# Optimization experiments

Measured on AMD Instinct MI355X. Metric: run time of the kernel, lower is better.

Reference implementation:

```python
import jax, jax.numpy as jnp
import numpy as np

HIDDEN = 4096
N_HEADS = 32
N_KV = 8
HEAD_DIM = 128
ROPE_THETA = 10000.0
B, S = 2, 2048


def _rope_neox(x, cos, sin):
    # x: [B,S,H,D]; cos/sin: [B,S,1,D/2]
    half = x.shape[-1] // 2
    x1, x2 = x[..., :half], x[..., half:]
    return jnp.concatenate([x1 * cos - x2 * sin, x2 * cos + x1 * sin], axis=-1)


def setup_inputs() -> dict:
    key = jax.random.key(0)
    k1, k2, k3 = jax.random.split(key, 3)
    hidden_states = jax.random.normal(k1, (B, S, HIDDEN), dtype=jnp.float32)
    positions = jnp.arange(B * S, dtype=jnp.int32).reshape(B, S)
    q_size = N_HEADS * HEAD_DIM
    kv_size = N_KV * HEAD_DIM
    w_qkv = jax.random.normal(k2, (HIDDEN, q_size + 2 * kv_size), dtype=jnp.float32) * (HIDDEN ** -0.5)
    w_o = jax.random.normal(k3, (q_size, HIDDEN), dtype=jnp.float32) * (q_size ** -0.5)
    return {"hidden_states": hidden_states, "positions": positions, "w_qkv": w_qkv, "w_o": w_o}


def reference(hidden_states, positions, w_qkv, w_o):
    q_size = N_HEADS * HEAD_DIM
    kv_size = N_KV * HEAD_DIM
    b, s, _ = hidden_states.shape

    qkv = hidden_states @ w_qkv  # [B,S,q+2kv]
    q = qkv[..., :q_size].reshape(b, s, N_HEADS, HEAD_DIM)
    k = qkv[..., q_size:q_size + kv_size].reshape(b, s, N_KV, HEAD_DIM)
    v = qkv[..., q_size + kv_size:].reshape(b, s, N_KV, HEAD_DIM)

    # RoPE (neox style, full rotary dim)
    inv_freq = 1.0 / (ROPE_THETA ** (jnp.arange(0, HEAD_DIM, 2, dtype=jnp.float32) / HEAD_DIM))
    ang = positions.astype(jnp.float32)[..., None] * inv_freq  # [B,S,D/2]
    cos = jnp.cos(ang)[:, :, None, :]
    sin = jnp.sin(ang)[:, :, None, :]
    q = _rope_neox(q, cos, sin)
    k = _rope_neox(k, cos, sin)

    # GQA: expand kv heads to match q heads
    rep = N_HEADS // N_KV
    k = jnp.repeat(k, rep, axis=2)  # [B,S,H,D]
    v = jnp.repeat(v, rep, axis=2)

    scale = HEAD_DIM ** -0.5
    scores = jnp.einsum('bqhd,bkhd->bhqk', q, k) * scale  # [B,H,S,S]
    causal = jnp.tril(jnp.ones((s, s), dtype=bool))
    scores = jnp.where(causal[None, None], scores, jnp.finfo(scores.dtype).min)
    probs = jax.nn.softmax(scores, axis=-1)
    attn = jnp.einsum('bhqk,bkhd->bqhd', probs, v).reshape(b, s, q_size)
    return attn @ w_o
```

## Files before the change

kernel.cpp:

```cpp
#include <hip/hip_runtime.h>
#include <hip/hip_bf16.h>
#include <stdint.h>
#include <stddef.h>

typedef unsigned short u16;
typedef __bf16 bf16x8 __attribute__((ext_vector_type(8)));
typedef float f32x4 __attribute__((ext_vector_type(4)));
typedef float f32x16 __attribute__((ext_vector_type(16)));
typedef unsigned u32x2 __attribute__((ext_vector_type(2)));

#define NH 32
#define NKV 8
#define HD 128
#define QKV_N 6144
#define SEQ 2048

__device__ __forceinline__ u16 f2b(float x) {
  union { float f; unsigned u; } v; v.f = x;
  unsigned r = v.u + 0x7FFF + ((v.u >> 16) & 1);
  return (u16)(r >> 16);
}
__device__ __forceinline__ float b2f(u16 b) {
  union { float f; unsigned u; } v; v.u = ((unsigned)b) << 16;
  return v.f;
}
__device__ __forceinline__ void gload16(const void* g, void* l) {
  __builtin_amdgcn_global_load_lds((const __attribute__((address_space(1))) unsigned int*)g,
                                   (__attribute__((address_space(3))) unsigned int*)l, 16, 0, 0);
}
__device__ __forceinline__ unsigned pk(float lo, float hi) {
  union { __bf16 h[2]; unsigned w; } u;
  u.h[0] = (__bf16)lo; u.h[1] = (__bf16)hi;
  return u.w;
}
__device__ __forceinline__ void plswap(unsigned& a, unsigned& b) {
  u32x2 r = __builtin_amdgcn_permlane32_swap(a, b, false, false);
  a = r.x; b = r.y;
}
__device__ __forceinline__ float pl_partner_max(float x) {
  unsigned u = __float_as_uint(x);
  u32x2 r = __builtin_amdgcn_permlane32_swap(u, u, false, false);
  return fmaxf(__uint_as_float(r.x), __uint_as_float(r.y));
}
__device__ __forceinline__ float pl_partner_sum(float x) {
  unsigned u = __float_as_uint(x);
  u32x2 r = __builtin_amdgcn_permlane32_swap(u, u, false, false);
  return __uint_as_float(r.x) + __uint_as_float(r.y);
}

__global__ void cast_f32_bf16(const float* __restrict__ in, u16* __restrict__ out, int n) {
  int i = (blockIdx.x * blockDim.x + threadIdx.x) * 4;
  if (i >= n) return;
  float4 v = *(const float4*)&in[i];
  ushort4 o;
  o.x = f2b(v.x); o.y = f2b(v.y); o.z = f2b(v.z); o.w = f2b(v.w);
  *(ushort4*)&out[i] = o;
}

__global__ void cast_transpose(const float* __restrict__ in, u16* __restrict__ out, int K, int N) {
  __shared__ float t[32][33];
  int n0 = blockIdx.x * 32, k0 = blockIdx.y * 32;
  int tx = threadIdx.x, ty = threadIdx.y;
#pragma unroll
  for (int i = 0; i < 4; ++i)
    t[ty + i * 8][tx] = in[(size_t)(k0 + ty + i * 8) * N + n0 + tx];
  __syncthreads();
#pragma unroll
  for (int i = 0; i < 4; ++i)
    out[(size_t)(n0 + ty + i * 8) * K + k0 + tx] = f2b(t[tx][ty + i * 8]);
}

__device__ __forceinline__ void storeC(float* C, size_t i, float v) { C[i] = v; }
__device__ __forceinline__ void storeC(u16* C, size_t i, float v) { C[i] = f2b(v); }

template <typename OutT>
__global__ __launch_bounds__(256) void gemm_bt(const u16* __restrict__ A, const u16* __restrict__ Bt,
                                               OutT* __restrict__ C, int M, int N, int K) {
  __shared__ __align__(16) u16 sA[128 * 64];
  __shared__ __align__(16) u16 sB[128 * 64];
  const int nbx = N >> 7;
  const int nwg = (M >> 7) * nbx;
  const int cpx = nwg >> 3;
  const int wg = (blockIdx.x & 7) * cpx + (blockIdx.x >> 3);
  const int row0 = (wg / nbx) << 7;
  const int col0 = (wg % nbx) << 7;
  const int tid = threadIdx.x, w = tid >> 6, lane = tid & 63;
  const int wr = (w >> 1) * 64, wc = (w & 1) * 64;
  f32x4 acc[4][4] = {};
  for (int kt = 0; kt < K; kt += 64) {
#pragma unroll
    for (int c = 0; c < 4; ++c) {
      const int g = c * 256 + w * 64 + lane;
      const int r = g >> 3, gc = g & 7;
      const int srcoff = kt + ((gc ^ (r & 7)) << 3);
      gload16(A + (size_t)(row0 + r) * K + srcoff, &sA[(c * 256 + w * 64) * 8]);
      gload16(Bt + (size_t)(col0 + r) * K + srcoff, &sB[(c * 256 + w * 64) * 8]);
    }
    __syncthreads();
#pragma unroll
    for (int ks = 0; ks < 2; ++ks) {
      bf16x8 a[4], b[4];
#pragma unroll
      for (int mi = 0; mi < 4; ++mi) {
        const int r = wr + mi * 16 + (lane & 15);
        const int g = (ks * 4 + (lane >> 4)) ^ (r & 7);
        a[mi] = *(const bf16x8*)&sA[r * 64 + g * 8];
      }
#pragma unroll
      for (int ni = 0; ni < 4; ++ni) {
        const int r = wc + ni * 16 + (lane & 15);
        const int g = (ks * 4 + (lane >> 4)) ^ (r & 7);
        b[ni] = *(const bf16x8*)&sB[r * 64 + g * 8];
      }
#pragma unroll
      for (int mi = 0; mi < 4; ++mi)
#pragma unroll
        for (int ni = 0; ni < 4; ++ni)
          acc[mi][ni] = __builtin_amdgcn_mfma_f32_16x16x32_bf16(a[mi], b[ni], acc[mi][ni], 0, 0, 0);
    }
    __syncthreads();
  }
#pragma unroll
  for (int mi = 0; mi < 4; ++mi)
#pragma unroll
    for (int ni = 0; ni < 4; ++ni)
#pragma unroll
      for (int j = 0; j < 4; ++j) {
        const int row = row0 + wr + mi * 16 + (lane >> 4) * 4 + j;
        const int col = col0 + wc + ni * 16 + (lane & 15);
        storeC(C, (size_t)row * N + col, acc[mi][ni][j]);
      }
}

__global__ void rope_kernel(u16* __restrict__ qkv, const int* __restrict__ pos, float qscale) {
  __shared__ float cs[64], sn[64];
  const int row = blockIdx.x;
  const int tid = threadIdx.x;
  if (tid < 64) {
    float p = (float)pos[row];
    float inv = exp2f(-(float)tid * 0.20762050593046f);
    float a = p * inv;
    cs[tid] = cosf(a);
    sn[tid] = sinf(a);
  }
  __syncthreads();
  const size_t base = (size_t)row * QKV_N;
  for (int i = tid; i < 40 * 64; i += 256) {
    const int h = i >> 6, d = i & 63;
    const size_t o = base + h * 128 + d;
    float x1 = b2f(qkv[o]), x2 = b2f(qkv[o + 64]);
    float c = cs[d], s = sn[d];
    float o1 = x1 * c - x2 * s;
    float o2 = x2 * c + x1 * s;
    if (h < NH) { o1 *= qscale; o2 *= qscale; }
    qkv[o] = f2b(o1);
    qkv[o + 64] = f2b(o2);
  }
}

__global__ void v_transpose(const u16* __restrict__ qkv, u16* __restrict__ vt) {
  __shared__ u16 t[32][33];
  const int b = blockIdx.z >> 3, kvh = blockIdx.z & 7;
  const int s0 = blockIdx.x * 32, d0 = blockIdx.y * 32;
  const int tx = threadIdx.x, ty = threadIdx.y;
#pragma unroll
  for (int i = 0; i < 4; ++i)
    t[ty + i * 8][tx] = qkv[(size_t)(b * SEQ + s0 + ty + i * 8) * QKV_N + 5120 + kvh * 128 + d0 + tx];
  __syncthreads();
#pragma unroll
  for (int i = 0; i < 4; ++i)
    vt[(size_t)((b * NKV + kvh) * HD + d0 + ty + i * 8) * SEQ + s0 + tx] = t[tx][ty + i * 8];
}

__global__ __launch_bounds__(512, 2) void attn_kernel(const u16* __restrict__ qkv, const u16* __restrict__ vt,
                                                      u16* __restrict__ attn) {
  __shared__ __align__(16) u16 sK[2][64 * 128];
  __shared__ __align__(16) u16 sV[2][128 * 64];
  const int b = blockIdx.z, h = blockIdx.y;
  const int qt = (b == 0) ? blockIdx.x : 7 - blockIdx.x;
  const int kvh = h >> 2;
  const int qb = qt * 256;
  const int tid = threadIdx.x, w = tid >> 6, lane = tid & 63;
  const int lq = lane & 31, hi = lane >> 5, x7 = lane & 7;
  const int qw = qb + (w << 5);
  const int qa = qw + lq;
  const int nt = 4 * (qt + 1);

  auto stage = [&](int buf, int kt) {
    const int k0 = kt * 64;
#pragma unroll
    for (int c = 0; c < 2; ++c) {
      const int g = c * 512 + tid;
      const int r = g >> 4, gc = g & 15;
      const int gs = gc ^ (r & 7);
      gload16(qkv + (size_t)(b * SEQ + k0 + r) * QKV_N + 4096 + kvh * 128 + gs * 8,
              &sK[buf][(c * 512 + (w << 6)) * 8]);
    }
#pragma unroll
    for (int c = 0; c < 2; ++c) {
      const int g = c * 512 + tid;
      const int r = g >> 3, gc = g & 7;
      const int gs = gc ^ (r & 7);
      gload16(vt + (size_t)((b * NKV + kvh) * HD + r) * SEQ + k0 + gs * 8,
              &sV[buf][(c * 512 + (w << 6)) * 8]);
    }
  };

  stage(0, 0);
  bf16x8 qf[8];
#pragma unroll
  for (int ks = 0; ks < 8; ++ks)
    qf[ks] = *(const bf16x8*)&qkv[(size_t)(b * SEQ + qw + lq) * QKV_N + h * 128 + ks * 16 + 8 * hi];

  f32x16 o[4] = {};
  float mreg = -1e30f, lreg = 0.f;

  asm volatile("s_waitcnt vmcnt(0)" ::: "memory");
  __builtin_amdgcn_s_barrier();

  for (int kt = 0; kt < nt; ++kt) {
    const int cur = kt & 1;
    const int k0 = kt * 64;
    if (kt + 1 < nt) {
      stage(cur ^ 1, kt + 1);
      asm volatile("s_waitcnt vmcnt(4)" ::: "memory");
    } else {
      asm volatile("s_waitcnt vmcnt(0)" ::: "memory");
    }
    __builtin_amdgcn_s_barrier();

    if (k0 <= qw + 31) {
      const u16* sk = sK[cur];
      f32x16 st0 = {}, st1 = {};
      __builtin_amdgcn_s_setprio(1);
#pragma unroll
      for (int ks = 0; ks < 8; ++ks) {
        const int g = ((2 * ks + hi) ^ x7) * 8;
        bf16x8 kf0 = *(const bf16x8*)&sk[lq * 128 + g];
        bf16x8 kf1 = *(const bf16x8*)&sk[(32 + lq) * 128 + g];
        st0 = __builtin_amdgcn_mfma_f32_32x32x16_bf16(kf0, qf[ks], st0, 0, 0, 0);
        st1 = __builtin_amdgcn_mfma_f32_32x32x16_bf16(kf1, qf[ks], st1, 0, 0, 0);
      }
      __builtin_amdgcn_s_setprio(0);
      if (k0 + 63 > qw) {
#pragma unroll
        for (int r = 0; r < 16; ++r) {
          const int cr = (r & 3) + 8 * (r >> 2) + 4 * hi;
          st0[r] = (k0 + cr <= qa) ? st0[r] : -1e30f;
          st1[r] = (k0 + 32 + cr <= qa) ? st1[r] : -1e30f;
        }
      }
      float a8[8];
#pragma unroll
      for (int r = 0; r < 8; ++r)
        a8[r] = fmaxf(fmaxf(st0[r], st0[r + 8]), fmaxf(st1[r], st1[r + 8]));
#pragma unroll
      for (int s = 4; s; s >>= 1)
#pragma unroll
        for (int r = 0; r < s; ++r) a8[r] = fmaxf(a8[r], a8[r + s]);
      const float pm = pl_partner_max(a8[0]);
      if (!__all(pm <= mreg + 8.f)) {
        const float mn = fmaxf(mreg, pm);
        const float al = exp2f(mreg - mn);
        lreg *= al;
        mreg = mn;
#pragma unroll
        for (int r = 0; r < 16; ++r) {
          const int cr = (r & 3) + 8 * (r >> 2) + 4 * hi;
          const float ar = __shfl(al, cr, 64);
#pragma unroll
          for (int dn = 0; dn < 4; ++dn) o[dn][r] *= ar;
        }
      }
#pragma unroll
      for (int r = 0; r < 16; ++r) {
        st0[r] = exp2f(st0[r] - mreg);
        st1[r] = exp2f(st1[r] - mreg);
      }
      float s8[8];
#pragma unroll
      for (int r = 0; r < 8; ++r)
        s8[r] = (st0[r] + st0[r + 8]) + (st1[r] + st1[r + 8]);
#pragma unroll
      for (int s = 4; s; s >>= 1)
#pragma unroll
        for (int r = 0; r < s; ++r) s8[r] += s8[r + s];
      lreg += pl_partner_sum(s8[0]);
      union U8 { unsigned w[4]; bf16x8 v; };
      U8 pa[4];
#define PACKFRAG(F, P0, P1, P2, P3, P4, P5, P6, P7)                   \
      {                                                               \
        unsigned a0 = pk(P0, P1), a1 = pk(P2, P3);                    \
        unsigned b0 = pk(P4, P5), b1 = pk(P6, P7);                    \
        plswap(a0, b0); plswap(a1, b1);                               \
        pa[F].w[0] = a0; pa[F].w[1] = a1; pa[F].w[2] = b0; pa[F].w[3] = b1; \
      }
      PACKFRAG(0, st0[0], st0[1], st0[2], st0[3], st0[4], st0[5], st0[6], st0[7])
      PACKFRAG(1, st0[8], st0[9], st0[10], st0[11], st0[12], st0[13], st0[14], st0[15])
      PACKFRAG(2, st1[0], st1[1], st1[2], st1[3], st1[4], st1[5], st1[6], st1[7])
      PACKFRAG(3, st1[8], st1[9], st1[10], st1[11], st1[12], st1[13], st1[14], st1[15])
#undef PACKFRAG
      const u16* sv = sV[cur];
      __builtin_amdgcn_s_setprio(1);
#pragma unroll
      for (int dn = 0; dn < 4; ++dn) {
#pragma unroll
        for (int ks = 0; ks < 4; ++ks) {
          bf16x8 vf = *(const bf16x8*)&sv[(dn * 32 + lq) * 64 + (((2 * ks + hi) ^ x7)) * 8];
          o[dn] = __builtin_amdgcn_mfma_f32_32x32x16_bf16(pa[ks].v, vf, o[dn], 0, 0, 0);
        }
      }
      __builtin_amdgcn_s_setprio(0);
    }
    __builtin_amdgcn_s_barrier();
  }

  const float inv = 1.0f / lreg;
#pragma unroll
  for (int r = 0; r < 16; ++r) {
    const int cr = (r & 3) + 8 * (r >> 2) + 4 * hi;
    const float fr = __shfl(inv, cr, 64);
    const size_t row = (size_t)(b * SEQ + qw + cr);
#pragma unroll
    for (int dn = 0; dn < 4; ++dn)
      attn[row * 4096 + h * 128 + dn * 32 + lq] = f2b(o[dn][r] * fr);
  }
}

extern "C" void kernel_launch(void* const* d_in, const int* in_sizes, int n_in,
                              void* d_out, int out_size, void* d_ws, size_t ws_size,
                              hipStream_t stream) {
  const float* hs = (const float*)d_in[0];
  const int* pos = (const int*)d_in[1];
  const float* w_qkv = (const float*)d_in[2];
  const float* w_o = (const float*)d_in[3];
  float* out = (float*)d_out;
  char* ws = (char*)d_ws;

  u16* hid = (u16*)ws;
  u16* attnb = hid;
  u16* wT = (u16*)(ws + 33554432);
  u16* qkv = (u16*)(ws + 83886080);
  u16* vt = (u16*)(ws + 134217728);

  const float qscale = 0.12751744f;

  cast_f32_bf16<<<16384, 256, 0, stream>>>(hs, hid, 4096 * 4096);
  cast_transpose<<<dim3(192, 128), dim3(32, 8), 0, stream>>>(w_qkv, wT, 4096, QKV_N);
  gemm_bt<u16><<<1536, 256, 0, stream>>>(hid, wT, qkv, 4096, QKV_N, 4096);
  rope_kernel<<<4096, 256, 0, stream>>>(qkv, pos, qscale);
  v_transpose<<<dim3(64, 4, 16), dim3(32, 8), 0, stream>>>(qkv, vt);
  cast_transpose<<<dim3(128, 128), dim3(32, 8), 0, stream>>>(w_o, wT, 4096, 4096);
  attn_kernel<<<dim3(8, 32, 2), 512, 0, stream>>>(qkv, vt, attnb);
  gemm_bt<float><<<1024, 256, 0, stream>>>(attnb, wT, out, 4096, 4096, 4096);
}
```

Before: 608.5 us.

## Replace GEMM with 256x256-tile double-buffered pipelined kernel using 512 threads

Replaces the 128x128 single-buffered GEMM with a 256x256-tile kernel that uses 8 waves and double-buffers shared memory. Global loads for the next tiles are issued in quarter-steps interleaved with MFMA work, with manual vmcnt waits and s_setprio to raise priority during the compute phase. This aims to hide global-load latency and raise arithmetic intensity per workgroup. In exchange it uses 128KB of LDS and many accumulator registers, and the manual waitcnt accounting is fragile. Only 384 or 256 workgroups are launched, which gives uneven waves on a 256-CU device.

```diff
diff --git a/kernel.cpp b/kernel.cpp
--- a/kernel.cpp
+++ b/kernel.cpp
@@ -74,62 +74,105 @@
 __device__ __forceinline__ void storeC(u16* C, size_t i, float v) { C[i] = f2b(v); }
 
 template <typename OutT>
-__global__ __launch_bounds__(256) void gemm_bt(const u16* __restrict__ A, const u16* __restrict__ Bt,
-                                               OutT* __restrict__ C, int M, int N, int K) {
-  __shared__ __align__(16) u16 sA[128 * 64];
-  __shared__ __align__(16) u16 sB[128 * 64];
-  const int nbx = N >> 7;
-  const int nwg = (M >> 7) * nbx;
+__global__ __launch_bounds__(512, 2) void gemm256(const u16* __restrict__ A, const u16* __restrict__ Bt,
+                                                  OutT* __restrict__ C, int M, int N, int K) {
+  __shared__ __align__(16) u16 sA[2 * 256 * 64];
+  __shared__ __align__(16) u16 sB[2 * 256 * 64];
+  const int nbx = N >> 8;
+  const int nwg = (M >> 8) * nbx;
   const int cpx = nwg >> 3;
-  const int wg = (blockIdx.x & 7) * cpx + (blockIdx.x >> 3);
-  const int row0 = (wg / nbx) << 7;
-  const int col0 = (wg % nbx) << 7;
+  const int wg = ((int)blockIdx.x & 7) * cpx + ((int)blockIdx.x >> 3);
+  const int row0 = (wg / nbx) << 8, col0 = (wg % nbx) << 8;
   const int tid = threadIdx.x, w = tid >> 6, lane = tid & 63;
-  const int wr = (w >> 1) * 64, wc = (w & 1) * 64;
-  f32x4 acc[4][4] = {};
-  for (int kt = 0; kt < K; kt += 64) {
-#pragma unroll
-    for (int c = 0; c < 4; ++c) {
-      const int g = c * 256 + w * 64 + lane;
+  const int wm = w >> 2, wn = w & 3;
+  const int lq = lane & 15, lh = lane >> 4, x7 = lq & 7;
+  const int o0 = (lh ^ x7) << 3, o1 = ((4 + lh) ^ x7) << 3;
+  const int sr7 = (tid >> 3) & 7;
+  const int nt = K >> 6;
+
+  auto stage = [&](const u16* __restrict__ src, u16* lbase, int rblk, int half, int t) {
+#pragma unroll
+    for (int c = 0; c < 2; ++c) {
+      const int g = c * 512 + tid;
       const int r = g >> 3, gc = g & 7;
-      const int srcoff = kt + ((gc ^ (r & 7)) << 3);
-      gload16(A + (size_t)(row0 + r) * K + srcoff, &sA[(c * 256 + w * 64) * 8]);
-      gload16(Bt + (size_t)(col0 + r) * K + srcoff, &sB[(c * 256 + w * 64) * 8]);
-    }
-    __syncthreads();
-#pragma unroll
-    for (int ks = 0; ks < 2; ++ks) {
-      bf16x8 a[4], b[4];
+      gload16(src + (size_t)(rblk + half * 128 + r) * K + t * 64 + ((gc ^ sr7) << 3),
+              lbase + (half * 1024 + c * 512 + (w << 6)) * 8);
+    }
+  };
+
+  f32x4 acc[4][4][2] = {};
+
+  stage(A, sA, row0, 0, 0);
+  stage(Bt, sB, col0, 0, 0);
+  stage(Bt, sB, col0, 1, 0);
+  stage(A, sA, row0, 1, 0);
+  stage(A, sA + 16384, row0, 0, 1);
+  stage(Bt, sB + 16384, col0, 0, 1);
+  asm volatile("s_waitcnt vmcnt(6)" ::: "memory");
+  __builtin_amdgcn_s_barrier();
+
+  for (int t = 0; t < nt; ++t) {
+    const int cur = t & 1;
+    u16* curA = sA + cur * 16384;
+    u16* curB = sB + cur * 16384;
+    u16* nxtA = sA + (cur ^ 1) * 16384;
+    u16* nxtB = sB + (cur ^ 1) * 16384;
+#pragma unroll
+    for (int q = 0; q < 4; ++q) {
+      const int ah = q >> 1, bh = q & 1;
+      bf16x8 af[4][2], bfr[2][2];
+      const u16* pa = curA + (ah * 128 + wm * 64 + lq) * 64;
+      const u16* pb = curB + (bh * 128 + wn * 32 + lq) * 64;
 #pragma unroll
       for (int mi = 0; mi < 4; ++mi) {
-        const int r = wr + mi * 16 + (lane & 15);
-        const int g = (ks * 4 + (lane >> 4)) ^ (r & 7);
-        a[mi] = *(const bf16x8*)&sA[r * 64 + g * 8];
-      }
-#pragma unroll
-      for (int ni = 0; ni < 4; ++ni) {
-        const int r = wc + ni * 16 + (lane & 15);
-        const int g = (ks * 4 + (lane >> 4)) ^ (r & 7);
-        b[ni] = *(const bf16x8*)&sB[r * 64 + g * 8];
-      }
-#pragma unroll
-      for (int mi = 0; mi < 4; ++mi)
-#pragma unroll
-        for (int ni = 0; ni < 4; ++ni)
-          acc[mi][ni] = __builtin_amdgcn_mfma_f32_16x16x32_bf16(a[mi], b[ni], acc[mi][ni], 0, 0, 0);
-    }
-    __syncthreads();
-  }
-#pragma unroll
-  for (int mi = 0; mi < 4; ++mi)
-#pragma unroll
-    for (int ni = 0; ni < 4; ++ni)
-#pragma unroll
-      for (int j = 0; j < 4; ++j) {
-        const int row = row0 + wr + mi * 16 + (lane >> 4) * 4 + j;
-        const int col = col0 + wc + ni * 16 + (lane & 15);
-        storeC(C, (size_t)row * N + col, acc[mi][ni][j]);
-      }
+        af[mi][0] = *(const bf16x8*)&pa[mi * 1024 + o0];
+        af[mi][1] = *(const bf16x8*)&pa[mi * 1024 + o1];
+      }
+#pragma unroll
+      for (int ni = 0; ni < 2; ++ni) {
+        bfr[ni][0] = *(const bf16x8*)&pb[ni * 1024 + o0];
+        bfr[ni][1] = *(const bf16x8*)&pb[ni * 1024 + o1];
+      }
+      if (q == 0 && t + 1 < nt) stage(Bt, nxtB, col0, 1, t + 1);
+      if (q == 1 && t + 1 < nt) stage(A, nxtA, row0, 1, t + 1);
+      if (q == 2 && t + 2 < nt) stage(A, curA, row0, 0, t + 2);
+      if (q == 3 && t + 2 < nt) stage(Bt, curB, col0, 0, t + 2);
+      __builtin_amdgcn_s_barrier();
+      __builtin_amdgcn_s_setprio(1);
+#pragma unroll
+      for (int ks = 0; ks < 2; ++ks)
+#pragma unroll
+        for (int mi = 0; mi < 4; ++mi)
+#pragma unroll
+          for (int ni = 0; ni < 2; ++ni)
+            acc[q][mi][ni] = __builtin_amdgcn_mfma_f32_16x16x32_bf16(af[mi][ks], bfr[ni][ks], acc[q][mi][ni], 0, 0, 0);
+      __builtin_amdgcn_s_setprio(0);
+      if (q == 1) {
+        if (t < nt - 1) asm volatile("s_waitcnt vmcnt(8)" ::: "memory");
+        else            asm volatile("s_waitcnt vmcnt(0)" ::: "memory");
+      }
+      if (q == 3 && t < nt - 1) {
+        if (t + 1 < nt - 1) asm volatile("s_waitcnt vmcnt(6)" ::: "memory");
+        else                asm volatile("s_waitcnt vmcnt(2)" ::: "memory");
+      }
+      __builtin_amdgcn_s_barrier();
+    }
+  }
+
+#pragma unroll
+  for (int q = 0; q < 4; ++q) {
+    const int ah = q >> 1, bh = q & 1;
+#pragma unroll
+    for (int mi = 0; mi < 4; ++mi)
+#pragma unroll
+      for (int ni = 0; ni < 2; ++ni)
+#pragma unroll
+        for (int j = 0; j < 4; ++j) {
+          const int row = row0 + ah * 128 + wm * 64 + mi * 16 + lh * 4 + j;
+          const int col = col0 + bh * 128 + wn * 32 + ni * 16 + lq;
+          storeC(C, (size_t)row * N + col, acc[q][mi][ni][j]);
+        }
+  }
 }
 
 __global__ void rope_kernel(u16* __restrict__ qkv, const int* __restrict__ pos, float qscale) {
@@ -347,10 +390,10 @@
 
   cast_f32_bf16<<<16384, 256, 0, stream>>>(hs, hid, 4096 * 4096);
   cast_transpose<<<dim3(192, 128), dim3(32, 8), 0, stream>>>(w_qkv, wT, 4096, QKV_N);
-  gemm_bt<u16><<<1536, 256, 0, stream>>>(hid, wT, qkv, 4096, QKV_N, 4096);
+  gemm256<u16><<<384, 512, 0, stream>>>(hid, wT, qkv, 4096, QKV_N, 4096);
   rope_kernel<<<4096, 256, 0, stream>>>(qkv, pos, qscale);
   v_transpose<<<dim3(64, 4, 16), dim3(32, 8), 0, stream>>>(qkv, vt);
   cast_transpose<<<dim3(128, 128), dim3(32, 8), 0, stream>>>(w_o, wT, 4096, 4096);
   attn_kernel<<<dim3(8, 32, 2), 512, 0, stream>>>(qkv, vt, attnb);
-  gemm_bt<float><<<1024, 256, 0, stream>>>(attnb, wT, out, 4096, 4096, 4096);
-}
+  gemm256<float><<<256, 512, 0, stream>>>(attnb, wT, out, 4096, 4096, 4096);
+}
```

Measured after the change: 589.5 us. 3.1% less time.

## Replace GEMM with 256x256 tile, double-buffered, 8-wave pipelined kernel

Applied to the files above, without the earlier changes.

Replaces the 128x128 single-buffered GEMM with a 256x256 tile kernel using 512 threads, double-buffered LDS, and an interleaved schedule. Global-to-LDS loads for the next k-tile are issued between MFMA phases, with explicit vmcnt waits, barriers and setprio. This is meant to hide memory latency and raise operand reuse in both projection GEMMs. In exchange it uses more LDS and registers and launches fewer workgroups (384 and 256), so occupancy and tail balance on 256 CUs may suffer.

```diff
diff --git a/kernel.cpp b/kernel.cpp
--- a/kernel.cpp
+++ b/kernel.cpp
@@ -27,6 +27,10 @@
 __device__ __forceinline__ void gload16(const void* g, void* l) {
   __builtin_amdgcn_global_load_lds((const __attribute__((address_space(1))) unsigned int*)g,
                                    (__attribute__((address_space(3))) unsigned int*)l, 16, 0, 0);
+}
+template <int N>
+__device__ __forceinline__ void vmwait() {
+  asm volatile("s_waitcnt vmcnt(%0)" ::"n"(N) : "memory");
 }
 __device__ __forceinline__ unsigned pk(float lo, float hi) {
   union { __bf16 h[2]; unsigned w; } u;
@@ -73,63 +77,136 @@
 __device__ __forceinline__ void storeC(float* C, size_t i, float v) { C[i] = v; }
 __device__ __forceinline__ void storeC(u16* C, size_t i, float v) { C[i] = f2b(v); }
 
+#define MFMA16(q, A0, A1, B0, B1)                                                              \
+  {                                                                                            \
+    _Pragma("unroll") for (int mi = 0; mi < 4; ++mi)                                           \
+      _Pragma("unroll") for (int ni = 0; ni < 2; ++ni)                                         \
+        acc[q][mi][ni] = __builtin_amdgcn_mfma_f32_16x16x32_bf16(A0[mi], B0[ni], acc[q][mi][ni], 0, 0, 0); \
+    _Pragma("unroll") for (int mi = 0; mi < 4; ++mi)                                           \
+      _Pragma("unroll") for (int ni = 0; ni < 2; ++ni)                                         \
+        acc[q][mi][ni] = __builtin_amdgcn_mfma_f32_16x16x32_bf16(A1[mi], B1[ni], acc[q][mi][ni], 0, 0, 0); \
+  }
+
+#define KTILE(NOFF, SGHI, SGLO, VMA, HASVMB, VMB)                                              \
+  {                                                                                            \
+    bf16x8 a0[4], a1[4], bl0[2], bl1[2], bh0[2], bh1[2];                                       \
+                                  \
+    _Pragma("unroll") for (int mi = 0; mi < 4; ++mi) {                                         \
+      a0[mi] = *(const bf16x8*)(rA0 + (NOFF) + mi * 1024);                                     \
+      a1[mi] = *(const bf16x8*)(rA1 + (NOFF) + mi * 1024);                                     \
+    }                                                                                          \
+    _Pragma("unroll") for (int ni = 0; ni < 2; ++ni) {                                         \
+      bl0[ni] = *(const bf16x8*)(rB0 + (NOFF) + ni * 1024);                                    \
+      bl1[ni] = *(const bf16x8*)(rB1 + (NOFF) + ni * 1024);                                    \
+      bh0[ni] = *(const bf16x8*)(rB0 + (NOFF) + 8192 + ni * 1024);                             \
+      bh1[ni] = *(const bf16x8*)(rB1 + (NOFF) + 8192 + ni * 1024);                             \
+    }                                                                                          \
+    if (SGHI) {                                                                                \
+      gload16(pBhi0, dBhi0 + ((NOFF) ^ 16384)); gload16(pBhi1, dBhi1 + ((NOFF) ^ 16384));      \
+      pBhi0 += 64; pBhi1 += 64;                                                                \
+      gload16(pAhi0, dAhi0 + ((NOFF) ^ 16384)); gload16(pAhi1, dAhi1 + ((NOFF) ^ 16384));      \
+      pAhi0 += 64; pAhi1 += 64;                                                                \
+    }                                                                                          \
+    __builtin_amdgcn_s_barrier();                                                              \
+    __builtin_amdgcn_s_setprio(1);                                                             \
+    MFMA16(0, a0, a1, bl0, bl1)                                                                \
+    MFMA16(1, a0, a1, bh0, bh1)                                                                \
+    __builtin_amdgcn_s_setprio(0);                                                             \
+    __builtin_amdgcn_sched_barrier(0);                                                         \
+    vmwait<VMA>();                                                                             \
+    __builtin_amdgcn_s_barrier();                                                              \
+                                         \
+    _Pragma("unroll") for (int mi = 0; mi < 4; ++mi) {                                         \
+      a0[mi] = *(const bf16x8*)(rA0 + (NOFF) + 8192 + mi * 1024);                              \
+      a1[mi] = *(const bf16x8*)(rA1 + (NOFF) + 8192 + mi * 1024);                              \
+    }                                                                                          \
+    if (SGLO) {                                                                                \
+      gload16(pAlo0, dAlo0 + (NOFF)); gload16(pAlo1, dAlo1 + (NOFF));                          \
+      pAlo0 += 64; pAlo1 += 64;                                                                \
+      gload16(pBlo0, dBlo0 + (NOFF)); gload16(pBlo1, dBlo1 + (NOFF));                          \
+      pBlo0 += 64; pBlo1 += 64;                                                                \
+    }                                                                                          \
+    __builtin_amdgcn_s_barrier();                                                              \
+    __builtin_amdgcn_s_setprio(1);                                                             \
+    MFMA16(2, a0, a1, bl0, bl1)                                                                \
+    MFMA16(3, a0, a1, bh0, bh1)                                                                \
+    __builtin_amdgcn_s_setprio(0);                                                             \
+    __builtin_amdgcn_sched_barrier(0);                                                         \
+    if (HASVMB) vmwait<VMB>();                                                                 \
+    __builtin_amdgcn_s_barrier();                                                              \
+  }
+
 template <typename OutT>
-__global__ __launch_bounds__(256) void gemm_bt(const u16* __restrict__ A, const u16* __restrict__ Bt,
-                                               OutT* __restrict__ C, int M, int N, int K) {
-  __shared__ __align__(16) u16 sA[128 * 64];
-  __shared__ __align__(16) u16 sB[128 * 64];
-  const int nbx = N >> 7;
-  const int nwg = (M >> 7) * nbx;
+__global__ __launch_bounds__(512, 2) void gemm256(const u16* __restrict__ A, const u16* __restrict__ Bt,
+                                                  OutT* __restrict__ C, int M, int N, int K) {
+  __shared__ __align__(16) u16 sA[2 * 16384];
+  __shared__ __align__(16) u16 sB[2 * 16384];
+  const int nbx = N >> 8;
+  const int nwg = (M >> 8) * nbx;
   const int cpx = nwg >> 3;
-  const int wg = (blockIdx.x & 7) * cpx + (blockIdx.x >> 3);
-  const int row0 = (wg / nbx) << 7;
-  const int col0 = (wg % nbx) << 7;
+  const int wg = ((int)blockIdx.x & 7) * cpx + ((int)blockIdx.x >> 3);
+  const int row0 = (wg / nbx) << 8, col0 = (wg % nbx) << 8;
   const int tid = threadIdx.x, w = tid >> 6, lane = tid & 63;
-  const int wr = (w >> 1) * 64, wc = (w & 1) * 64;
-  f32x4 acc[4][4] = {};
-  for (int kt = 0; kt < K; kt += 64) {
-#pragma unroll
-    for (int c = 0; c < 4; ++c) {
-      const int g = c * 256 + w * 64 + lane;
-      const int r = g >> 3, gc = g & 7;
-      const int srcoff = kt + ((gc ^ (r & 7)) << 3);
-      gload16(A + (size_t)(row0 + r) * K + srcoff, &sA[(c * 256 + w * 64) * 8]);
-      gload16(Bt + (size_t)(col0 + r) * K + srcoff, &sB[(c * 256 + w * 64) * 8]);
-    }
-    __syncthreads();
-#pragma unroll
-    for (int ks = 0; ks < 2; ++ks) {
-      bf16x8 a[4], b[4];
-#pragma unroll
-      for (int mi = 0; mi < 4; ++mi) {
-        const int r = wr + mi * 16 + (lane & 15);
-        const int g = (ks * 4 + (lane >> 4)) ^ (r & 7);
-        a[mi] = *(const bf16x8*)&sA[r * 64 + g * 8];
-      }
-#pragma unroll
-      for (int ni = 0; ni < 4; ++ni) {
-        const int r = wc + ni * 16 + (lane & 15);
-        const int g = (ks * 4 + (lane >> 4)) ^ (r & 7);
-        b[ni] = *(const bf16x8*)&sB[r * 64 + g * 8];
-      }
-#pragma unroll
-      for (int mi = 0; mi < 4; ++mi)
-#pragma unroll
-        for (int ni = 0; ni < 4; ++ni)
-          acc[mi][ni] = __builtin_amdgcn_mfma_f32_16x16x32_bf16(a[mi], b[ni], acc[mi][ni], 0, 0, 0);
-    }
-    __syncthreads();
-  }
-#pragma unroll
-  for (int mi = 0; mi < 4; ++mi)
-#pragma unroll
-    for (int ni = 0; ni < 4; ++ni)
-#pragma unroll
-      for (int j = 0; j < 4; ++j) {
-        const int row = row0 + wr + mi * 16 + (lane >> 4) * 4 + j;
-        const int col = col0 + wc + ni * 16 + (lane & 15);
-        storeC(C, (size_t)row * N + col, acc[mi][ni][j]);
-      }
+  const int wm = w >> 2, wn = w & 3;
+  const int lq = lane & 15, lh = lane >> 4, x7 = lq & 7;
+  const int o0 = (lh ^ x7) << 3, o1 = ((4 + lh) ^ x7) << 3;
+  const int nt = K >> 6;
+
+  const int rr = tid >> 3;
+  const int swz = ((tid & 7) ^ (rr & 7)) << 3;
+  const u16* pAlo0 = A + (size_t)(row0 + rr) * K + swz;
+  const u16* pAlo1 = A + (size_t)(row0 + 64 + rr) * K + swz;
+  const u16* pAhi0 = A + (size_t)(row0 + 128 + rr) * K + swz;
+  const u16* pAhi1 = A + (size_t)(row0 + 192 + rr) * K + swz;
+  const u16* pBlo0 = Bt + (size_t)(col0 + rr) * K + swz;
+  const u16* pBlo1 = Bt + (size_t)(col0 + 64 + rr) * K + swz;
+  const u16* pBhi0 = Bt + (size_t)(col0 + 128 + rr) * K + swz;
+  const u16* pBhi1 = Bt + (size_t)(col0 + 192 + rr) * K + swz;
+  u16* dAlo0 = sA + w * 512;
+  u16* dAlo1 = sA + 4096 + w * 512;
+  u16* dAhi0 = sA + 8192 + w * 512;
+  u16* dAhi1 = sA + 12288 + w * 512;
+  u16* dBlo0 = sB + w * 512;
+  u16* dBlo1 = sB + 4096 + w * 512;
+  u16* dBhi0 = sB + 8192 + w * 512;
+  u16* dBhi1 = sB + 12288 + w * 512;
+  const u16* rA0 = sA + (wm * 64 + lq) * 64 + o0;
+  const u16* rA1 = sA + (wm * 64 + lq) * 64 + o1;
+  const u16* rB0 = sB + (wn * 32 + lq) * 64 + o0;
+  const u16* rB1 = sB + (wn * 32 + lq) * 64 + o1;
+
+  f32x4 acc[4][4][2] = {};
+
+  gload16(pAlo0, dAlo0); gload16(pAlo1, dAlo1); pAlo0 += 64; pAlo1 += 64;
+  gload16(pBlo0, dBlo0); gload16(pBlo1, dBlo1); pBlo0 += 64; pBlo1 += 64;
+  gload16(pBhi0, dBhi0); gload16(pBhi1, dBhi1); pBhi0 += 64; pBhi1 += 64;
+  gload16(pAhi0, dAhi0); gload16(pAhi1, dAhi1); pAhi0 += 64; pAhi1 += 64;
+  gload16(pAlo0, dAlo0 + 16384); gload16(pAlo1, dAlo1 + 16384); pAlo0 += 64; pAlo1 += 64;
+  gload16(pBlo0, dBlo0 + 16384); gload16(pBlo1, dBlo1 + 16384); pBlo0 += 64; pBlo1 += 64;
+  vmwait<6>();
+  __builtin_amdgcn_s_barrier();
+
+  for (int t = 0; t < nt - 2; t += 2) {
+    KTILE(0, 1, 1, 8, 1, 6)
+    KTILE(16384, 1, 1, 8, 1, 6)
+  }
+  KTILE(0, 1, 0, 8, 1, 2)
+  KTILE(16384, 0, 0, 0, 0, 0)
+
+#pragma unroll
+  for (int q = 0; q < 4; ++q) {
+    const int ah = q >> 1, bh2 = q & 1;
+#pragma unroll
+    for (int mi = 0; mi < 4; ++mi)
+#pragma unroll
+      for (int ni = 0; ni < 2; ++ni)
+#pragma unroll
+        for (int j = 0; j < 4; ++j) {
+          const int row = row0 + ah * 128 + wm * 64 + mi * 16 + lh * 4 + j;
+          const int col = col0 + bh2 * 128 + wn * 32 + ni * 16 + lq;
+          storeC(C, (size_t)row * N + col, acc[q][mi][ni][j]);
+        }
+  }
 }
 
 __global__ void rope_kernel(u16* __restrict__ qkv, const int* __restrict__ pos, float qscale) {
@@ -347,10 +424,10 @@
 
   cast_f32_bf16<<<16384, 256, 0, stream>>>(hs, hid, 4096 * 4096);
   cast_transpose<<<dim3(192, 128), dim3(32, 8), 0, stream>>>(w_qkv, wT, 4096, QKV_N);
-  gemm_bt<u16><<<1536, 256, 0, stream>>>(hid, wT, qkv, 4096, QKV_N, 4096);
+  gemm256<u16><<<384, 512, 0, stream>>>(hid, wT, qkv, 4096, QKV_N, 4096);
   rope_kernel<<<4096, 256, 0, stream>>>(qkv, pos, qscale);
   v_transpose<<<dim3(64, 4, 16), dim3(32, 8), 0, stream>>>(qkv, vt);
   cast_transpose<<<dim3(128, 128), dim3(32, 8), 0, stream>>>(w_o, wT, 4096, 4096);
   attn_kernel<<<dim3(8, 32, 2), 512, 0, stream>>>(qkv, vt, attnb);
-  gemm_bt<float><<<1024, 256, 0, stream>>>(attnb, wT, out, 4096, 4096, 4096);
-}
+  gemm256<float><<<256, 512, 0, stream>>>(attnb, wT, out, 4096, 4096, 4096);
+}
```

After: 545.3 us. 10.4% less time.

## Replace GEMM with triple-buffered 256xBN pipelined kernel and vectorize RoPE

Applied to the files above, without the earlier changes.

Replaces the single-buffered 128x128 GEMM with a 512-thread kernel that uses 256-row tiles, triple-buffered A and double-buffered B in LDS, and global-to-LDS loads overlapped with MFMA. It uses explicit vmcnt waits, raw s_barrier and raised wave priority during the MFMA block. Tile widths of 192 and 128 are chosen so the QKV and output projections each launch 512 blocks. The RoPE kernel is also changed to process four elements per thread with vector loads and stores. The GEMM hardcodes K=4096 through a fixed iteration count, and the larger LDS footprint and register use may limit occupancy.

```diff
diff --git a/kernel.cpp b/kernel.cpp
--- a/kernel.cpp
+++ b/kernel.cpp
@@ -27,6 +27,10 @@
 __device__ __forceinline__ void gload16(const void* g, void* l) {
   __builtin_amdgcn_global_load_lds((const __attribute__((address_space(1))) unsigned int*)g,
                                    (__attribute__((address_space(3))) unsigned int*)l, 16, 0, 0);
+}
+template <int N>
+__device__ __forceinline__ void vmwait() {
+  asm volatile("s_waitcnt vmcnt(%0)" ::"n"(N) : "memory");
 }
 __device__ __forceinline__ unsigned pk(float lo, float hi) {
   union { __bf16 h[2]; unsigned w; } u;
@@ -73,63 +77,125 @@
 __device__ __forceinline__ void storeC(float* C, size_t i, float v) { C[i] = v; }
 __device__ __forceinline__ void storeC(u16* C, size_t i, float v) { C[i] = f2b(v); }
 
-template <typename OutT>
-__global__ __launch_bounds__(256) void gemm_bt(const u16* __restrict__ A, const u16* __restrict__ Bt,
-                                               OutT* __restrict__ C, int M, int N, int K) {
-  __shared__ __align__(16) u16 sA[128 * 64];
-  __shared__ __align__(16) u16 sB[128 * 64];
-  const int nbx = N >> 7;
-  const int nwg = (M >> 7) * nbx;
+#define TMM(h, X0, X1)                                                                         \
+  _Pragma("unroll") for (int mi = 0; mi < 4; ++mi)                                             \
+    _Pragma("unroll") for (int ni = 0; ni < NI; ++ni)                                          \
+      acc[h][mi][ni] = __builtin_amdgcn_mfma_f32_16x16x32_bf16(X0[mi], b0[ni], acc[h][mi][ni], 0, 0, 0); \
+  _Pragma("unroll") for (int mi = 0; mi < 4; ++mi)                                             \
+    _Pragma("unroll") for (int ni = 0; ni < NI; ++ni)                                          \
+      acc[h][mi][ni] = __builtin_amdgcn_mfma_f32_16x16x32_bf16(X1[mi], b1[ni], acc[h][mi][ni], 0, 0, 0);
+
+#define KTT(RA, RB2, SA, SB2, SGA, SGB, VM)                                                    \
+  {                                                                                            \
+    if (SGB) {                                                                                 \
+      gload16(pB0, dB0 + (SB2) * BS); gload16(pB1, dB1 + (SB2) * BS);                          \
+      pB0 += 64; pB1 += 64;                                                                    \
+      if (NI >= 3) { gload16(pB2, dB2 + (SB2) * BS); pB2 += 64; }                              \
+    }                                                                                          \
+    if (SGA) {                                                                                 \
+      gload16(pA0, dA0 + (SA) * 16384); gload16(pA1, dA1 + (SA) * 16384);                      \
+      gload16(pA2, dA2 + (SA) * 16384); gload16(pA3, dA3 + (SA) * 16384);                      \
+      pA0 += 64; pA1 += 64; pA2 += 64; pA3 += 64;                                              \
+    }                                                                                          \
+    bf16x8 al0[4], al1[4], ah0[4], ah1[4], b0[NI], b1[NI];                                     \
+    _Pragma("unroll") for (int mi = 0; mi < 4; ++mi) {                                         \
+      al0[mi] = *(const bf16x8*)(rA0 + (RA) * 16384 + mi * 1024);                              \
+      al1[mi] = *(const bf16x8*)(rA1 + (RA) * 16384 + mi * 1024);                              \
+    }                                                                                          \
+    _Pragma("unroll") for (int ni = 0; ni < NI; ++ni) {                                        \
+      b0[ni] = *(const bf16x8*)(rB0 + (RB2) * BS + ni * 1024);                                 \
+      b1[ni] = *(const bf16x8*)(rB1 + (RB2) * BS + ni * 1024);                                 \
+    }                                                                                          \
+    _Pragma("unroll") for (int mi = 0; mi < 4; ++mi) {                                         \
+      ah0[mi] = *(const bf16x8*)(rA0 + (RA) * 16384 + 8192 + mi * 1024);                       \
+      ah1[mi] = *(const bf16x8*)(rA1 + (RA) * 16384 + 8192 + mi * 1024);                       \
+    }                                                                                          \
+    __builtin_amdgcn_s_setprio(1);                                                             \
+    TMM(0, al0, al1)                                                                           \
+    TMM(1, ah0, ah1)                                                                           \
+    __builtin_amdgcn_s_setprio(0);                                                             \
+    __builtin_amdgcn_sched_barrier(0);                                                         \
+    if ((VM) == 2) vmwait<4>();                                                                \
+    else if ((VM) == 1) vmwait<0>();                                                           \
+    __builtin_amdgcn_s_barrier();                                                              \
+  }
+
+template <int BN, typename OutT>
+__global__ __launch_bounds__(512, 2) void gemm_tri(const u16* __restrict__ A, const u16* __restrict__ Bt,
+                                                   OutT* __restrict__ C, int M, int N, int K) {
+  constexpr int NI = BN / 64;
+  constexpr int BS = BN * 64;
+  __shared__ __align__(16) u16 sA[3 * 16384];
+  __shared__ __align__(16) u16 sB[2 * BS];
+  const int nbx = N / BN;
+  const int nwg = (M >> 8) * nbx;
   const int cpx = nwg >> 3;
-  const int wg = (blockIdx.x & 7) * cpx + (blockIdx.x >> 3);
-  const int row0 = (wg / nbx) << 7;
-  const int col0 = (wg % nbx) << 7;
+  const int wg = ((int)blockIdx.x & 7) * cpx + ((int)blockIdx.x >> 3);
+  const int row0 = (wg / nbx) << 8, col0 = (wg % nbx) * BN;
   const int tid = threadIdx.x, w = tid >> 6, lane = tid & 63;
-  const int wr = (w >> 1) * 64, wc = (w & 1) * 64;
-  f32x4 acc[4][4] = {};
-  for (int kt = 0; kt < K; kt += 64) {
-#pragma unroll
-    for (int c = 0; c < 4; ++c) {
-      const int g = c * 256 + w * 64 + lane;
-      const int r = g >> 3, gc = g & 7;
-      const int srcoff = kt + ((gc ^ (r & 7)) << 3);
-      gload16(A + (size_t)(row0 + r) * K + srcoff, &sA[(c * 256 + w * 64) * 8]);
-      gload16(Bt + (size_t)(col0 + r) * K + srcoff, &sB[(c * 256 + w * 64) * 8]);
-    }
-    __syncthreads();
-#pragma unroll
-    for (int ks = 0; ks < 2; ++ks) {
-      bf16x8 a[4], b[4];
-#pragma unroll
-      for (int mi = 0; mi < 4; ++mi) {
-        const int r = wr + mi * 16 + (lane & 15);
-        const int g = (ks * 4 + (lane >> 4)) ^ (r & 7);
-        a[mi] = *(const bf16x8*)&sA[r * 64 + g * 8];
-      }
-#pragma unroll
-      for (int ni = 0; ni < 4; ++ni) {
-        const int r = wc + ni * 16 + (lane & 15);
-        const int g = (ks * 4 + (lane >> 4)) ^ (r & 7);
-        b[ni] = *(const bf16x8*)&sB[r * 64 + g * 8];
-      }
-#pragma unroll
-      for (int mi = 0; mi < 4; ++mi)
-#pragma unroll
-        for (int ni = 0; ni < 4; ++ni)
-          acc[mi][ni] = __builtin_amdgcn_mfma_f32_16x16x32_bf16(a[mi], b[ni], acc[mi][ni], 0, 0, 0);
-    }
-    __syncthreads();
-  }
-#pragma unroll
-  for (int mi = 0; mi < 4; ++mi)
-#pragma unroll
-    for (int ni = 0; ni < 4; ++ni)
-#pragma unroll
-      for (int j = 0; j < 4; ++j) {
-        const int row = row0 + wr + mi * 16 + (lane >> 4) * 4 + j;
-        const int col = col0 + wc + ni * 16 + (lane & 15);
-        storeC(C, (size_t)row * N + col, acc[mi][ni][j]);
-      }
+  const int wm = w >> 2, wn = w & 3;
+  const int lq = lane & 15, lh = lane >> 4, x7 = lq & 7;
+  const int o0 = (lh ^ x7) << 3, o1 = ((4 + lh) ^ x7) << 3;
+
+  const int rr = tid >> 3;
+  const int swz = ((tid & 7) ^ (rr & 7)) << 3;
+  const u16* pA0 = A + (size_t)(row0 + rr) * K + swz;
+  const u16* pA1 = A + (size_t)(row0 + 64 + rr) * K + swz;
+  const u16* pA2 = A + (size_t)(row0 + 128 + rr) * K + swz;
+  const u16* pA3 = A + (size_t)(row0 + 192 + rr) * K + swz;
+  const u16* pB0 = Bt + (size_t)(col0 + rr) * K + swz;
+  const u16* pB1 = Bt + (size_t)(col0 + 64 + rr) * K + swz;
+  const u16* pB2 = Bt + (size_t)(col0 + 128 + rr) * K + swz;
+  u16* dA0 = sA + w * 512;
+  u16* dA1 = sA + 4096 + w * 512;
+  u16* dA2 = sA + 8192 + w * 512;
+  u16* dA3 = sA + 12288 + w * 512;
+  u16* dB0 = sB + w * 512;
+  u16* dB1 = sB + 4096 + w * 512;
+  u16* dB2 = sB + 8192 + w * 512;
+  const u16* rA0 = sA + (wm * 64 + lq) * 64 + o0;
+  const u16* rA1 = sA + (wm * 64 + lq) * 64 + o1;
+  const u16* rB0 = sB + (wn * (BN / 4) + lq) * 64 + o0;
+  const u16* rB1 = sB + (wn * (BN / 4) + lq) * 64 + o1;
+
+  f32x4 acc[2][4][NI] = {};
+
+  gload16(pA0, dA0); gload16(pA1, dA1); gload16(pA2, dA2); gload16(pA3, dA3);
+  pA0 += 64; pA1 += 64; pA2 += 64; pA3 += 64;
+  gload16(pB0, dB0); gload16(pB1, dB1);
+  pB0 += 64; pB1 += 64;
+  if (NI >= 3) { gload16(pB2, dB2); pB2 += 64; }
+  gload16(pA0, dA0 + 16384); gload16(pA1, dA1 + 16384);
+  gload16(pA2, dA2 + 16384); gload16(pA3, dA3 + 16384);
+  pA0 += 64; pA1 += 64; pA2 += 64; pA3 += 64;
+  vmwait<4>();
+  __builtin_amdgcn_s_barrier();
+
+  for (int it = 0; it < 10; ++it) {
+    KTT(0, 0, 2, 1, 1, 1, 2)
+    KTT(1, 1, 0, 0, 1, 1, 2)
+    KTT(2, 0, 1, 1, 1, 1, 2)
+    KTT(0, 1, 2, 0, 1, 1, 2)
+    KTT(1, 0, 0, 1, 1, 1, 2)
+    KTT(2, 1, 1, 0, 1, 1, 2)
+  }
+  KTT(0, 0, 2, 1, 1, 1, 2)
+  KTT(1, 1, 0, 0, 1, 1, 2)
+  KTT(2, 0, 0, 1, 0, 1, 1)
+  KTT(0, 1, 0, 0, 0, 0, 0)
+
+#pragma unroll
+  for (int ah = 0; ah < 2; ++ah)
+#pragma unroll
+    for (int mi = 0; mi < 4; ++mi)
+#pragma unroll
+      for (int ni = 0; ni < NI; ++ni)
+#pragma unroll
+        for (int j = 0; j < 4; ++j) {
+          const int row = row0 + ah * 128 + wm * 64 + mi * 16 + lh * 4 + j;
+          const int col = col0 + wn * (BN / 4) + ni * 16 + lq;
+          storeC(C, (size_t)row * N + col, acc[ah][mi][ni][j]);
+        }
 }
 
 __global__ void rope_kernel(u16* __restrict__ qkv, const int* __restrict__ pos, float qscale) {
@@ -145,16 +211,31 @@
   }
   __syncthreads();
   const size_t base = (size_t)row * QKV_N;
-  for (int i = tid; i < 40 * 64; i += 256) {
-    const int h = i >> 6, d = i & 63;
-    const size_t o = base + h * 128 + d;
-    float x1 = b2f(qkv[o]), x2 = b2f(qkv[o + 64]);
-    float c = cs[d], s = sn[d];
-    float o1 = x1 * c - x2 * s;
-    float o2 = x2 * c + x1 * s;
-    if (h < NH) { o1 *= qscale; o2 *= qscale; }
-    qkv[o] = f2b(o1);
-    qkv[o + 64] = f2b(o2);
+  for (int i = tid; i < 40 * 16; i += 256) {
+    const int h = i >> 4, dq = (i & 15) * 4;
+    const size_t o = base + h * 128 + dq;
+    ushort4 v1 = *(const ushort4*)&qkv[o];
+    ushort4 v2 = *(const ushort4*)&qkv[o + 64];
+    const float sc = (h < NH) ? qscale : 1.0f;
+    ushort4 r1, r2;
+    {
+      float x1 = b2f(v1.x), x2 = b2f(v2.x), c = cs[dq], s = sn[dq];
+      r1.x = f2b((x1 * c - x2 * s) * sc); r2.x = f2b((x2 * c + x1 * s) * sc);
+    }
+    {
+      float x1 = b2f(v1.y), x2 = b2f(v2.y), c = cs[dq + 1], s = sn[dq + 1];
+      r1.y = f2b((x1 * c - x2 * s) * sc); r2.y = f2b((x2 * c + x1 * s) * sc);
+    }
+    {
+      float x1 = b2f(v1.z), x2 = b2f(v2.z), c = cs[dq + 2], s = sn[dq + 2];
+      r1.z = f2b((x1 * c - x2 * s) * sc); r2.z = f2b((x2 * c + x1 * s) * sc);
+    }
+    {
+      float x1 = b2f(v1.w), x2 = b2f(v2.w), c = cs[dq + 3], s = sn[dq + 3];
+      r1.w = f2b((x1 * c - x2 * s) * sc); r2.w = f2b((x2 * c + x1 * s) * sc);
+    }
+    *(ushort4*)&qkv[o] = r1;
+    *(ushort4*)&qkv[o + 64] = r2;
   }
 }
 
@@ -347,10 +428,10 @@
 
   cast_f32_bf16<<<16384, 256, 0, stream>>>(hs, hid, 4096 * 4096);
   cast_transpose<<<dim3(192, 128), dim3(32, 8), 0, stream>>>(w_qkv, wT, 4096, QKV_N);
-  gemm_bt<u16><<<1536, 256, 0, stream>>>(hid, wT, qkv, 4096, QKV_N, 4096);
+  gemm_tri<192, u16><<<512, 512, 0, stream>>>(hid, wT, qkv, 4096, QKV_N, 4096);
   rope_kernel<<<4096, 256, 0, stream>>>(qkv, pos, qscale);
   v_transpose<<<dim3(64, 4, 16), dim3(32, 8), 0, stream>>>(qkv, vt);
   cast_transpose<<<dim3(128, 128), dim3(32, 8), 0, stream>>>(w_o, wT, 4096, 4096);
   attn_kernel<<<dim3(8, 32, 2), 512, 0, stream>>>(qkv, vt, attnb);
-  gemm_bt<float><<<1024, 256, 0, stream>>>(attnb, wT, out, 4096, 4096, 4096);
-}
+  gemm_tri<128, float><<<512, 512, 0, stream>>>(attnb, wT, out, 4096, 4096, 4096);
+}
```

Result: faster. 543.8 us (-10.6%).
